# Kernel tuning notes

Hardware: AMD Instinct MI355X
Metric: run time of the kernel (lower is better)

Reference implementation:

```python
import jax, jax.numpy as jnp
import numpy as np
import math

N_LAYERS = 6
F = 512   # num_feature
H = 8     # num_head
DH = F // H
V = 32000 # vocab size
B = 64
S = 512   # == PositionalEncoding max_len
EPS = 1e-5


def _make_pe(max_len, d_model):
    position = np.arange(max_len, dtype=np.float32)[:, None]
    div_term = np.exp(np.arange(0, d_model, 2, dtype=np.float32) * (-math.log(10000.0) / d_model))
    pe = np.zeros((max_len, d_model), dtype=np.float32)
    pe[:, 0::2] = np.sin(position * div_term)
    pe[:, 1::2] = np.cos(position * div_term)
    return jnp.asarray(pe)


def setup_inputs() -> dict:
    key = jax.random.key(0)
    ks = jax.random.split(key, 16)
    w = lambda k, shape, s=0.02: (jax.random.normal(k, shape, dtype=jnp.float32) * s)
    inp = {
        "text": jax.random.randint(ks[0], (B, S), 0, V),
        "emb": jax.random.normal(ks[1], (V, F), dtype=jnp.float32) * 0.25,
        "pe": _make_pe(S, F),
        # per-layer params stacked on leading N axis
        "Wq": w(ks[2], (N_LAYERS, F, F)), "bq": jnp.zeros((N_LAYERS, F), jnp.float32),
        "Wk": w(ks[3], (N_LAYERS, F, F)), "bk": jnp.zeros((N_LAYERS, F), jnp.float32),
        "Wv": w(ks[4], (N_LAYERS, F, F)), "bv": jnp.zeros((N_LAYERS, F), jnp.float32),
        "g1": jnp.ones((N_LAYERS, F), jnp.float32), "beta1": jnp.zeros((N_LAYERS, F), jnp.float32),
        "Wf": w(ks[5], (N_LAYERS, F, F)), "bf": jnp.zeros((N_LAYERS, F), jnp.float32),
        "g2": jnp.ones((N_LAYERS, F), jnp.float32), "beta2": jnp.zeros((N_LAYERS, F), jnp.float32),
    }
    return inp


def _layernorm(x, g, b):
    m = jnp.mean(x, axis=-1, keepdims=True)
    v = jnp.mean(jnp.square(x - m), axis=-1, keepdims=True)
    return (x - m) * jax.lax.rsqrt(v + EPS) * g + b


def _encoder_layer(x, Wq, bq, Wk, bk, Wv, bv, g1, beta1, Wf, bf, g2, beta2):
    Bz, Sz, Fz = x.shape
    q = (x @ Wq + bq).reshape(Bz, Sz, H, DH)
    k = (x @ Wk + bk).reshape(Bz, Sz, H, DH)
    v = (x @ Wv + bv).reshape(Bz, Sz, H, DH)
    # FAITHFUL to source bug: attention over HEADS per token, no 1/sqrt(d) scaling.
    score = jnp.einsum('bshd,bsgd->bshg', q, k)          # [B,S,H,H]
    weight = jax.nn.softmax(score, axis=-1)
    attn = jnp.einsum('bshg,bsgd->bshd', weight, v).reshape(Bz, Sz, Fz)
    x = _layernorm(attn + x, g1, beta1)
    x = _layernorm((x @ Wf + bf) + x, g2, beta2)
    return x


def reference(text, emb, pe, Wq, bq, Wk, bk, Wv, bv, g1, beta1, Wf, bf, g2, beta2):
    x = emb[text] + pe[None, :text.shape[1], :]  # embedding + pos-enc (dropout = eval identity)
    for i in range(N_LAYERS):
        x = _encoder_layer(x, Wq[i], bq[i], Wk[i], bk[i], Wv[i], bv[i],
                           g1[i], beta1[i], Wf[i], bf[i], g2[i], beta2[i])
    return x
```

## Files before the change

### kernel.cpp

```cpp
#include <hip/hip_runtime.h>
#include <stdint.h>

typedef unsigned short u16;
using frag8 = __attribute__((ext_vector_type(8))) short;
using f32x4 = __attribute__((ext_vector_type(4))) float;

#define NTOK 32768
#define FDIM 512

__device__ __forceinline__ float bflo(uint32_t p){ union{uint32_t u; float f;} v; v.u = p<<16; return v.f; }
__device__ __forceinline__ float bfhi(uint32_t p){ union{uint32_t u; float f;} v; v.u = p & 0xffff0000u; return v.f; }
__device__ __forceinline__ float bf1(u16 x){ union{uint32_t u; float f;} v; v.u = ((uint32_t)x)<<16; return v.f; }
__device__ __forceinline__ u16 f2bf(float f){
  union{float f; uint32_t u;} v; v.f = f;
  uint32_t u = v.u;
  u += 0x7fffu + ((u>>16)&1u);
  return (u16)(u>>16);
}

__device__ __forceinline__ void async16(const void* g, void* l){
  __builtin_amdgcn_global_load_lds((const __attribute__((address_space(1))) uint32_t*)g,
                                   (__attribute__((address_space(3))) uint32_t*)l, 16, 0, 0);
}

__global__ __launch_bounds__(256) void embed_kernel(const int* __restrict__ text,
    const float* __restrict__ emb, const float* __restrict__ pe,
    u16* __restrict__ xb, const int tok0){
  const int gid = blockIdx.x*256 + threadIdx.x;
  const int base = gid*4;
  const int tl = base >> 9;
  const int f  = base & 511;
  const int tg = tl + tok0;
  const int s  = tg & 511;
  const int tok = text[tg];
  const float4 e4 = *(const float4*)(emb + (size_t)tok*FDIM + f);
  const float4 p4 = *(const float4*)(pe  + (size_t)s*FDIM + f);
  ushort4 ob;
  ob.x = f2bf(e4.x + p4.x);
  ob.y = f2bf(e4.y + p4.y);
  ob.z = f2bf(e4.z + p4.z);
  ob.w = f2bf(e4.w + p4.w);
  *(ushort4*)(xb + base) = ob;
}

__global__ __launch_bounds__(256) void transpose_w(const float* __restrict__ Wq,
    const float* __restrict__ Wk, const float* __restrict__ Wv, const float* __restrict__ Wf,
    u16* __restrict__ WT){
  const int gid = blockIdx.x*256 + threadIdx.x;
  const int n   = gid & 2047;
  const int k8  = (gid>>11) & 63;
  const int lay = gid >> 17;
  const float* src; int col;
  if      (n <  512){ src = Wq; col = n;      }
  else if (n < 1024){ src = Wk; col = n-512;  }
  else if (n < 1536){ src = Wv; col = n-1024; }
  else              { src = Wf; col = n-1536; }
  src += (size_t)lay*FDIM*FDIM;
  u16 vals[8] __attribute__((aligned(16)));
  #pragma unroll
  for (int i=0;i<8;i++) vals[i] = f2bf(src[(size_t)(k8*8+i)*FDIM + col]);
  *(int4*)(WT + ((size_t)lay*2048 + n)*FDIM + k8*8) = *(const int4*)vals;
}

template<int MODE>
__global__ __launch_bounds__(256, 3) void gemm128(
    const u16* __restrict__ A, const u16* __restrict__ BT,
    const float* __restrict__ b0, const float* __restrict__ b1, const float* __restrict__ b2,
    const u16* __restrict__ resid, u16* __restrict__ C, const int ldC, const int NB){
  __shared__ __attribute__((aligned(16))) short As[3*128*32];
  __shared__ __attribute__((aligned(16))) short Bs[3*128*32];
  const int nwg = gridDim.x;
  const int orig = blockIdx.x;
  const int wg = ((nwg & 7) == 0) ? ((orig & 7)*(nwg >> 3) + (orig >> 3)) : orig;
  const int nblk = wg % NB, mblk = wg / NB;
  const int m0 = mblk << 7, n0 = nblk << 7;
  const int tid = threadIdx.x;
  const int wid = tid >> 6, l = tid & 63;
  const int lm = l & 15, quad = l >> 4;

  const int srow = wid*16 + (l >> 2);
  const int sch  = (l & 3) ^ ((l >> 3) & 3);
  const char* Asrc0 = (const char*)A  + ((size_t)(m0 + srow))*1024 + sch*16;
  const char* Asrc1 = Asrc0 + 64*1024;
  const char* Bsrc0 = (const char*)BT + ((size_t)(n0 + srow))*1024 + sch*16;
  const char* Bsrc1 = Bsrc0 + 64*1024;
  char* ldsAw = (char*)As + wid*1024;
  char* ldsBw = (char*)Bs + wid*1024;

  f32x4 acc[4][4];
  #pragma unroll
  for (int i=0;i<4;i++)
    #pragma unroll
    for (int j=0;j<4;j++){ f32x4 z = {0.f,0.f,0.f,0.f}; acc[i][j] = z; }

  const int rsel = quad ^ ((lm >> 1) & 3);
  const int aB = ((wid>>1)*64 + lm)*32 + rsel*8;
  const int bB = ((wid&1)*64  + lm)*32 + rsel*8;

  #pragma unroll
  for (int kt=0; kt<2; kt++){
    async16(Asrc0 + kt*64, ldsAw + kt*8192);
    async16(Asrc1 + kt*64, ldsAw + kt*8192 + 4096);
    async16(Bsrc0 + kt*64, ldsBw + kt*8192);
    async16(Bsrc1 + kt*64, ldsBw + kt*8192 + 4096);
  }

#define TILE(T_, DOSTAGE, VMC) { \
    asm volatile("s_waitcnt vmcnt(" #VMC ")" ::: "memory"); \
    __builtin_amdgcn_s_barrier(); \
    asm volatile("" ::: "memory"); \
    if (DOSTAGE){ const int s_ = ((T_)+2)%3; const int off_ = ((T_)+2)*64; \
      async16(Asrc0 + off_, ldsAw + s_*8192); \
      async16(Asrc1 + off_, ldsAw + s_*8192 + 4096); } \
    const short* sA_ = As + ((T_)%3)*4096; \
    const short* sB_ = Bs + ((T_)%3)*4096; \
    frag8 af_[4], bf_[4]; \
    _Pragma("unroll") \
    for (int x_=0;x_<4;x_++) af_[x_] = *(const frag8*)(sA_ + aB + x_*512); \
    _Pragma("unroll") \
    for (int x_=0;x_<4;x_++) bf_[x_] = *(const frag8*)(sB_ + bB + x_*512); \
    if (DOSTAGE){ const int s_ = ((T_)+2)%3; const int off_ = ((T_)+2)*64; \
      async16(Bsrc0 + off_, ldsBw + s_*8192); \
      async16(Bsrc1 + off_, ldsBw + s_*8192 + 4096); } \
    __builtin_amdgcn_s_setprio(1); \
    _Pragma("unroll") \
    for (int mi_=0;mi_<4;mi_++) \
      _Pragma("unroll") \
      for (int nj_=0;nj_<4;nj_++) \
        acc[mi_][nj_] = __builtin_amdgcn_mfma_f32_16x16x32_bf16(af_[mi_], bf_[nj_], acc[mi_][nj_], 0,0,0); \
    __builtin_amdgcn_s_setprio(0); }

  TILE(0,1,4)  TILE(1,1,4)  TILE(2,1,4)  TILE(3,1,4)
  TILE(4,1,4)  TILE(5,1,4)  TILE(6,1,4)  TILE(7,1,4)
  TILE(8,1,4)  TILE(9,1,4)  TILE(10,1,4) TILE(11,1,4)
  TILE(12,1,4) TILE(13,1,4) TILE(14,0,4) TILE(15,0,0)
#undef TILE

  float bias[4]; int cols[4];
  #pragma unroll
  for (int nj=0;nj<4;nj++){
    const int c = n0 + (wid&1)*64 + nj*16 + lm;
    cols[nj] = c;
    if (MODE==0) bias[nj] = (c<512 ? b0[c] : (c<1024 ? b1[c-512] : b2[c-1024]));
    else         bias[nj] = b0[c];
  }
  #pragma unroll
  for (int mi=0; mi<4; mi++){
    const int rbase = m0 + (wid>>1)*64 + mi*16 + quad*4;
    #pragma unroll
    for (int r=0;r<4;r++){
      const size_t row = (size_t)(rbase + r);
      #pragma unroll
      for (int nj=0;nj<4;nj++){
        float v = acc[mi][nj][r] + bias[nj];
        if (MODE==1) v += bf1(resid[row*FDIM + cols[nj]]);
        C[row*(size_t)ldC + cols[nj]] = f2bf(v);
      }
    }
  }
}

__global__ __launch_bounds__(256) void attn_ln1(const u16* __restrict__ qkvb,
    const u16* __restrict__ xb, const float* __restrict__ gam, const float* __restrict__ bet,
    u16* __restrict__ y1b){
  __shared__ __attribute__((aligned(16))) u16 sQ[4][1536];
  __shared__ float sWt[4][64];
  const int tid = threadIdx.x, w = tid>>6, l = tid&63;
  const int t = blockIdx.x*4 + w;
  {
    const int4* src = (const int4*)(qkvb + (size_t)t*1536);
    int4* dst = (int4*)(&sQ[w][0]);
    #pragma unroll
    for (int i=0;i<3;i++) dst[i*64 + l] = src[i*64 + l];
  }
  __syncthreads();
  const int h = l>>3, g = l&7;
  const u16* qrow = &sQ[w][h*64];
  const u16* krow = &sQ[w][512 + g*64];
  float sc = 0.f;
  const int dstart = (l&31)*2;
  #pragma unroll
  for (int i=0;i<32;i++){
    const int d = (dstart + 2*i) & 63;
    const uint32_t qp = *(const uint32_t*)(qrow + d);
    const uint32_t kp = *(const uint32_t*)(krow + d);
    sc += bflo(qp)*bflo(kp) + bfhi(qp)*bfhi(kp);
  }
  float mx = sc;
  mx = fmaxf(mx, __shfl_xor(mx,1));
  mx = fmaxf(mx, __shfl_xor(mx,2));
  mx = fmaxf(mx, __shfl_xor(mx,4));
  const float e = __expf(sc - mx);
  float ssum = e;
  ssum += __shfl_xor(ssum,1);
  ssum += __shfl_xor(ssum,2);
  ssum += __shfl_xor(ssum,4);
  sWt[w][l] = e / ssum;
  __syncthreads();
  float wt[8];
  #pragma unroll
  for (int gg=0;gg<8;gg++) wt[gg] = sWt[w][h*8+gg];
  float att[8] = {0,0,0,0,0,0,0,0};
  const int d0 = (l&7)*8;
  #pragma unroll
  for (int gg=0;gg<8;gg++){
    const int4 vv = *(const int4*)(&sQ[w][1024 + gg*64 + d0]);
    const uint32_t* vp = (const uint32_t*)&vv;
    #pragma unroll
    for (int p=0;p<4;p++){
      att[2*p]   += wt[gg]*bflo(vp[p]);
      att[2*p+1] += wt[gg]*bfhi(vp[p]);
    }
  }
  const size_t rb = (size_t)t*FDIM + l*8;
  const int4 xv = *(const int4*)(xb + rb);
  const uint32_t* xp = (const uint32_t*)&xv;
  float y[8]; float s1=0.f, s2=0.f;
  #pragma unroll
  for (int p=0;p<4;p++){
    y[2*p]   = att[2*p]   + bflo(xp[p]);
    y[2*p+1] = att[2*p+1] + bfhi(xp[p]);
  }
  #pragma unroll
  for (int j=0;j<8;j++){ s1 += y[j]; s2 += y[j]*y[j]; }
  #pragma unroll
  for (int off=1; off<64; off<<=1){ s1 += __shfl_xor(s1,off); s2 += __shfl_xor(s2,off); }
  const float mean = s1*(1.f/512.f);
  const float var  = s2*(1.f/512.f) - mean*mean;
  const float rstd = rsqrtf(var + 1e-5f);
  const float4 g0 = *(const float4*)(gam + l*8);
  const float4 g1v = *(const float4*)(gam + l*8 + 4);
  const float4 b0v = *(const float4*)(bet + l*8);
  const float4 b1v = *(const float4*)(bet + l*8 + 4);
  float of[8];
  of[0]=(y[0]-mean)*rstd*g0.x + b0v.x;
  of[1]=(y[1]-mean)*rstd*g0.y + b0v.y;
  of[2]=(y[2]-mean)*rstd*g0.z + b0v.z;
  of[3]=(y[3]-mean)*rstd*g0.w + b0v.w;
  of[4]=(y[4]-mean)*rstd*g1v.x + b1v.x;
  of[5]=(y[5]-mean)*rstd*g1v.y + b1v.y;
  of[6]=(y[6]-mean)*rstd*g1v.z + b1v.z;
  of[7]=(y[7]-mean)*rstd*g1v.w + b1v.w;
  u16 ob[8] __attribute__((aligned(16)));
  #pragma unroll
  for (int j=0;j<8;j++) ob[j] = f2bf(of[j]);
  *(int4*)(y1b + rb) = *(const int4*)ob;
}

__global__ __launch_bounds__(256) void ln2_kernel(const u16* __restrict__ z,
    const float* __restrict__ gam, const float* __restrict__ bet,
    u16* __restrict__ xb, float* __restrict__ outp, const int final_){
  const int tid = threadIdx.x, w = tid>>6, l = tid&63;
  const int t = blockIdx.x*4 + w;
  const size_t rb = (size_t)t*FDIM + l*8;
  const int4 zv = *(const int4*)(z + rb);
  const uint32_t* zp = (const uint32_t*)&zv;
  float y[8];
  #pragma unroll
  for (int p=0;p<4;p++){ y[2*p]=bflo(zp[p]); y[2*p+1]=bfhi(zp[p]); }
  float s1=0.f, s2=0.f;
  #pragma unroll
  for (int j=0;j<8;j++){ s1+=y[j]; s2+=y[j]*y[j]; }
  #pragma unroll
  for (int off=1; off<64; off<<=1){ s1 += __shfl_xor(s1,off); s2 += __shfl_xor(s2,off); }
  const float mean = s1*(1.f/512.f);
  const float var  = s2*(1.f/512.f) - mean*mean;
  const float rstd = rsqrtf(var + 1e-5f);
  const float4 g0 = *(const float4*)(gam + l*8);
  const float4 g1v = *(const float4*)(gam + l*8 + 4);
  const float4 b0v = *(const float4*)(bet + l*8);
  const float4 b1v = *(const float4*)(bet + l*8 + 4);
  float of[8];
  of[0]=(y[0]-mean)*rstd*g0.x + b0v.x;
  of[1]=(y[1]-mean)*rstd*g0.y + b0v.y;
  of[2]=(y[2]-mean)*rstd*g0.z + b0v.z;
  of[3]=(y[3]-mean)*rstd*g0.w + b0v.w;
  of[4]=(y[4]-mean)*rstd*g1v.x + b1v.x;
  of[5]=(y[5]-mean)*rstd*g1v.y + b1v.y;
  of[6]=(y[6]-mean)*rstd*g1v.z + b1v.z;
  of[7]=(y[7]-mean)*rstd*g1v.w + b1v.w;
  if (final_){
    float4 o0; o0.x=of[0]; o0.y=of[1]; o0.z=of[2]; o0.w=of[3];
    float4 o1; o1.x=of[4]; o1.y=of[5]; o1.z=of[6]; o1.w=of[7];
    *(float4*)(outp + rb) = o0;
    *(float4*)(outp + rb + 4) = o1;
  } else {
    u16 ob[8] __attribute__((aligned(16)));
    #pragma unroll
    for (int j=0;j<8;j++) ob[j] = f2bf(of[j]);
    *(int4*)(xb + rb) = *(const int4*)ob;
  }
}

extern "C" void kernel_launch(void* const* d_in, const int* in_sizes, int n_in,
                              void* d_out, int out_size, void* d_ws, size_t ws_size,
                              hipStream_t stream){
  const int*   text = (const int*)d_in[0];
  const float* emb = (const float*)d_in[1];
  const float* pe  = (const float*)d_in[2];
  const float* Wq  = (const float*)d_in[3];
  const float* bq  = (const float*)d_in[4];
  const float* Wk  = (const float*)d_in[5];
  const float* bk  = (const float*)d_in[6];
  const float* Wv  = (const float*)d_in[7];
  const float* bv  = (const float*)d_in[8];
  const float* g1  = (const float*)d_in[9];
  const float* be1 = (const float*)d_in[10];
  const float* Wf  = (const float*)d_in[11];
  const float* bf_ = (const float*)d_in[12];
  const float* g2  = (const float*)d_in[13];
  const float* be2 = (const float*)d_in[14];
  float* outp = (float*)d_out;

  const size_t wtB = (size_t)6*2048*512*2;
  int T = NTOK;
  while (T > 2048 && wtB + (size_t)T*5120 > ws_size) T >>= 1;

  char* ws = (char*)d_ws;
  u16*   WT  = (u16*)ws;
  char*  act = ws + wtB;
  u16*   xb  = (u16*)act;
  u16*   y1b = (u16*)(act + (size_t)T*1024);
  u16*   qkv = (u16*)(act + (size_t)T*2048);
  u16*   zb  = qkv;

  hipLaunchKernelGGL(transpose_w, dim3(3072), dim3(256), 0, stream, Wq, Wk, Wv, Wf, WT);

  const int chunks = NTOK / T;
  for (int c = 0; c < chunks; c++){
    const int tok0 = c*T;
    hipLaunchKernelGGL(embed_kernel, dim3(T/2), dim3(256), 0, stream, text, emb, pe, xb, tok0);
    for (int lay=0; lay<6; lay++){
      const u16* WTl = WT + (size_t)lay*2048*FDIM;
      hipLaunchKernelGGL((gemm128<0>), dim3((T/128)*12), dim3(256), 0, stream,
          xb, WTl, bq + lay*FDIM, bk + lay*FDIM, bv + lay*FDIM, (const u16*)nullptr, qkv, 1536, 12);
      hipLaunchKernelGGL(attn_ln1, dim3(T/4), dim3(256), 0, stream,
          qkv, xb, g1 + lay*FDIM, be1 + lay*FDIM, y1b);
      hipLaunchKernelGGL((gemm128<1>), dim3((T/128)*4), dim3(256), 0, stream,
          y1b, WTl + (size_t)1536*FDIM, bf_ + lay*FDIM, (const float*)nullptr, (const float*)nullptr,
          y1b, zb, 512, 4);
      hipLaunchKernelGGL(ln2_kernel, dim3(T/4), dim3(256), 0, stream,
          zb, g2 + lay*FDIM, be2 + lay*FDIM, xb, outp + (size_t)tok0*FDIM, (lay==5)?1:0);
    }
  }
}
```

Baseline: 968.7 us.

## Replace 128x128 GEMM with 256x256 eight-wave ping-pong tiled kernel

Replaces the 128x128, 4-wave, triple-buffered GEMM with a 256x256 tile run by 512 threads (8 waves, each computing 128x64). It uses 128 KB of LDS double-buffered over K=64 steps, and interleaves quarter-tile LDS reads, async global-to-LDS staging and MFMA bursts between barriers. The larger tile raises arithmetic intensity and cuts global traffic per FLOP. The cost is more barriers, a larger LDS footprint limiting occupancy, and fewer workgroups for the N=512 GEMM (T/256*2 blocks), which may underfill the GPU.

Result: faster. 882.8 us (-8.9%).

```diff
diff --git a/kernel.cpp b/kernel.cpp
--- a/kernel.cpp
+++ b/kernel.cpp
@@ -63,90 +63,112 @@
 }
 
 template<int MODE>
-__global__ __launch_bounds__(256, 3) void gemm128(
+__global__ __launch_bounds__(512, 2) void gemm8p(
     const u16* __restrict__ A, const u16* __restrict__ BT,
     const float* __restrict__ b0, const float* __restrict__ b1, const float* __restrict__ b2,
     const u16* __restrict__ resid, u16* __restrict__ C, const int ldC, const int NB){
-  __shared__ __attribute__((aligned(16))) short As[3*128*32];
-  __shared__ __attribute__((aligned(16))) short Bs[3*128*32];
+  __shared__ __attribute__((aligned(16))) char lds[131072];
   const int nwg = gridDim.x;
   const int orig = blockIdx.x;
-  const int wg = ((nwg & 7) == 0) ? ((orig & 7)*(nwg >> 3) + (orig >> 3)) : orig;
+  const int wg = ((nwg & 7)==0) ? ((orig&7)*(nwg>>3) + (orig>>3)) : orig;
   const int nblk = wg % NB, mblk = wg / NB;
-  const int m0 = mblk << 7, n0 = nblk << 7;
+  const int m0 = mblk<<8, n0 = nblk<<8;
   const int tid = threadIdx.x;
-  const int wid = tid >> 6, l = tid & 63;
-  const int lm = l & 15, quad = l >> 4;
-
-  const int srow = wid*16 + (l >> 2);
-  const int sch  = (l & 3) ^ ((l >> 3) & 3);
-  const char* Asrc0 = (const char*)A  + ((size_t)(m0 + srow))*1024 + sch*16;
-  const char* Asrc1 = Asrc0 + 64*1024;
-  const char* Bsrc0 = (const char*)BT + ((size_t)(n0 + srow))*1024 + sch*16;
-  const char* Bsrc1 = Bsrc0 + 64*1024;
-  char* ldsAw = (char*)As + wid*1024;
-  char* ldsBw = (char*)Bs + wid*1024;
-
-  f32x4 acc[4][4];
-  #pragma unroll
-  for (int i=0;i<4;i++)
+  const int wid = tid>>6, l = tid&63;
+  const int lm = l&15, quad = l>>4;
+  const int wm = wid>>2, wn = wid&3;
+
+  const int cg = (l&3) ^ ((l>>3)&3);
+  const char* aSrc = (const char*)A  + ((size_t)(m0 + (wid>>2)*128 + (wid&3)*16 + (l>>2)))*1024 + cg*16;
+  const char* bSrc = (const char*)BT + ((size_t)(n0 + (wid>>1)*64  + (wid&1)*16 + (l>>2)))*1024 + cg*16;
+  char* ldsAs = lds + wid*1024;
+  char* ldsBs = lds + 65536 + wid*1024;
+
+#define STGA(kt, kw, mh) async16(aSrc + (mh)*65536 + (kt)*128 + (kw)*64, \
+                                 ldsAs + (((kt)&1)*32768) + (kw)*16384 + (mh)*8192)
+#define STGB(kt, kw, nh) async16(bSrc + (nh)*32768 + (kt)*128 + (kw)*64, \
+                                 ldsBs + (((kt)&1)*32768) + (kw)*16384 + (nh)*8192)
+
+  f32x4 acc[8][4];
+  #pragma unroll
+  for (int i=0;i<8;i++)
     #pragma unroll
     for (int j=0;j<4;j++){ f32x4 z = {0.f,0.f,0.f,0.f}; acc[i][j] = z; }
 
-  const int rsel = quad ^ ((lm >> 1) & 3);
-  const int aB = ((wid>>1)*64 + lm)*32 + rsel*8;
-  const int bB = ((wid&1)*64  + lm)*32 + rsel*8;
-
-  #pragma unroll
-  for (int kt=0; kt<2; kt++){
-    async16(Asrc0 + kt*64, ldsAw + kt*8192);
-    async16(Asrc1 + kt*64, ldsAw + kt*8192 + 4096);
-    async16(Bsrc0 + kt*64, ldsBw + kt*8192);
-    async16(Bsrc1 + kt*64, ldsBw + kt*8192 + 4096);
-  }
-
-#define TILE(T_, DOSTAGE, VMC) { \
-    asm volatile("s_waitcnt vmcnt(" #VMC ")" ::: "memory"); \
-    __builtin_amdgcn_s_barrier(); \
-    asm volatile("" ::: "memory"); \
-    if (DOSTAGE){ const int s_ = ((T_)+2)%3; const int off_ = ((T_)+2)*64; \
-      async16(Asrc0 + off_, ldsAw + s_*8192); \
-      async16(Asrc1 + off_, ldsAw + s_*8192 + 4096); } \
-    const short* sA_ = As + ((T_)%3)*4096; \
-    const short* sB_ = Bs + ((T_)%3)*4096; \
-    frag8 af_[4], bf_[4]; \
-    _Pragma("unroll") \
-    for (int x_=0;x_<4;x_++) af_[x_] = *(const frag8*)(sA_ + aB + x_*512); \
-    _Pragma("unroll") \
-    for (int x_=0;x_<4;x_++) bf_[x_] = *(const frag8*)(sB_ + bB + x_*512); \
-    if (DOSTAGE){ const int s_ = ((T_)+2)%3; const int off_ = ((T_)+2)*64; \
-      async16(Bsrc0 + off_, ldsBw + s_*8192); \
-      async16(Bsrc1 + off_, ldsBw + s_*8192 + 4096); } \
-    __builtin_amdgcn_s_setprio(1); \
-    _Pragma("unroll") \
-    for (int mi_=0;mi_<4;mi_++) \
-      _Pragma("unroll") \
-      for (int nj_=0;nj_<4;nj_++) \
-        acc[mi_][nj_] = __builtin_amdgcn_mfma_f32_16x16x32_bf16(af_[mi_], bf_[nj_], acc[mi_][nj_], 0,0,0); \
-    __builtin_amdgcn_s_setprio(0); }
-
-  TILE(0,1,4)  TILE(1,1,4)  TILE(2,1,4)  TILE(3,1,4)
-  TILE(4,1,4)  TILE(5,1,4)  TILE(6,1,4)  TILE(7,1,4)
-  TILE(8,1,4)  TILE(9,1,4)  TILE(10,1,4) TILE(11,1,4)
-  TILE(12,1,4) TILE(13,1,4) TILE(14,0,4) TILE(15,0,0)
-#undef TILE
+  const int csw = (quad ^ ((l>>1)&3))*16;
+  const char* aRd = lds + wm*4096 + lm*64 + csw;
+  const char* bRd = lds + 65536 + wn*2048 + lm*64 + csw;
+
+  frag8 a[4][2], bR[2][2][2];
+
+  STGA(0,0,0); STGA(0,1,0); STGB(0,0,0); STGB(0,1,0); STGB(0,0,1); STGB(0,1,1); STGA(0,0,1); STGA(0,1,1);
+  STGA(1,0,0); STGA(1,1,0); STGB(1,0,0); STGB(1,1,0); STGB(1,0,1); STGB(1,1,1);
+  asm volatile("s_waitcnt vmcnt(6)" ::: "memory");
+  __builtin_amdgcn_s_barrier();
+
+#define RDA(BUF, MH) { _Pragma("unroll") for (int mi_=0;mi_<4;mi_++){ \
+    a[mi_][0] = *(const frag8*)(aRd + (BUF)*32768 + (MH)*8192 + mi_*1024); \
+    a[mi_][1] = *(const frag8*)(aRd + (BUF)*32768 + 16384 + (MH)*8192 + mi_*1024); } }
+#define RDB(BUF, NH) { _Pragma("unroll") for (int nj_=0;nj_<2;nj_++){ \
+    bR[NH][nj_][0] = *(const frag8*)(bRd + (BUF)*32768 + (NH)*8192 + nj_*1024); \
+    bR[NH][nj_][1] = *(const frag8*)(bRd + (BUF)*32768 + 16384 + (NH)*8192 + nj_*1024); } }
+#define MM(MH, NH) { __builtin_amdgcn_s_setprio(1); \
+  _Pragma("unroll") for (int kw_=0;kw_<2;kw_++) \
+  _Pragma("unroll") for (int mi_=0;mi_<4;mi_++) \
+  _Pragma("unroll") for (int nj_=0;nj_<2;nj_++) \
+    acc[(MH)*4+mi_][(NH)*2+nj_] = __builtin_amdgcn_mfma_f32_16x16x32_bf16( \
+        a[mi_][kw_], bR[NH][nj_][kw_], acc[(MH)*4+mi_][(NH)*2+nj_], 0,0,0); \
+  __builtin_amdgcn_s_setprio(0); }
+#define BAR __builtin_amdgcn_s_barrier()
+
+#define ITER(T, FULL) { \
+   RDA(((T)&1),0); RDB(((T)&1),0); STGA((T)+1,0,1); STGA((T)+1,1,1); \
+           BAR; MM(0,0); BAR; \
+   RDB(((T)&1),1); if (FULL){ STGA((T)+2,0,0); STGA((T)+2,1,0); } \
+           BAR; MM(0,1); BAR; \
+   RDA(((T)&1),1); if (FULL){ STGB((T)+2,0,0); STGB((T)+2,1,0); } \
+           BAR; MM(1,0); BAR; \
+   if (FULL){ STGB((T)+2,0,1); STGB((T)+2,1,1); } \
+           BAR; MM(1,1); \
+           if (FULL){ asm volatile("s_waitcnt vmcnt(6)" ::: "memory"); } \
+           else     { asm volatile("s_waitcnt vmcnt(0)" ::: "memory"); } \
+           BAR; \
+   RDA((((T)+1)&1),0); RDB((((T)+1)&1),0); if (FULL){ STGA((T)+2,0,1); STGA((T)+2,1,1); } \
+           BAR; MM(0,0); BAR; \
+   RDB((((T)+1)&1),1); if (FULL){ STGA((T)+3,0,0); STGA((T)+3,1,0); } \
+           BAR; MM(0,1); BAR; \
+   RDA((((T)+1)&1),1); if (FULL){ STGB((T)+3,0,0); STGB((T)+3,1,0); } \
+           BAR; MM(1,0); BAR; \
+   if (FULL){ STGB((T)+3,0,1); STGB((T)+3,1,1); } \
+           BAR; MM(1,1); \
+           if (FULL){ asm volatile("s_waitcnt vmcnt(6)" ::: "memory"); } \
+           BAR; \
+}
+
+  ITER(0,1)
+  ITER(2,1)
+  ITER(4,1)
+  ITER(6,0)
+
+#undef ITER
+#undef BAR
+#undef MM
+#undef RDB
+#undef RDA
+#undef STGB
+#undef STGA
 
   float bias[4]; int cols[4];
   #pragma unroll
   for (int nj=0;nj<4;nj++){
-    const int c = n0 + (wid&1)*64 + nj*16 + lm;
+    const int c = n0 + wn*64 + nj*16 + lm;
     cols[nj] = c;
     if (MODE==0) bias[nj] = (c<512 ? b0[c] : (c<1024 ? b1[c-512] : b2[c-1024]));
     else         bias[nj] = b0[c];
   }
   #pragma unroll
-  for (int mi=0; mi<4; mi++){
-    const int rbase = m0 + (wid>>1)*64 + mi*16 + quad*4;
+  for (int mi=0; mi<8; mi++){
+    const int rbase = m0 + wm*128 + mi*16 + quad*4;
     #pragma unroll
     for (int r=0;r<4;r++){
       const size_t row = (size_t)(rbase + r);
@@ -332,13 +354,13 @@
     hipLaunchKernelGGL(embed_kernel, dim3(T/2), dim3(256), 0, stream, text, emb, pe, xb, tok0);
     for (int lay=0; lay<6; lay++){
       const u16* WTl = WT + (size_t)lay*2048*FDIM;
-      hipLaunchKernelGGL((gemm128<0>), dim3((T/128)*12), dim3(256), 0, stream,
-          xb, WTl, bq + lay*FDIM, bk + lay*FDIM, bv + lay*FDIM, (const u16*)nullptr, qkv, 1536, 12);
+      hipLaunchKernelGGL((gemm8p<0>), dim3((T/256)*6), dim3(512), 0, stream,
+          xb, WTl, bq + lay*FDIM, bk + lay*FDIM, bv + lay*FDIM, (const u16*)nullptr, qkv, 1536, 6);
       hipLaunchKernelGGL(attn_ln1, dim3(T/4), dim3(256), 0, stream,
           qkv, xb, g1 + lay*FDIM, be1 + lay*FDIM, y1b);
-      hipLaunchKernelGGL((gemm128<1>), dim3((T/128)*4), dim3(256), 0, stream,
+      hipLaunchKernelGGL((gemm8p<1>), dim3((T/256)*2), dim3(512), 0, stream,
           y1b, WTl + (size_t)1536*FDIM, bf_ + lay*FDIM, (const float*)nullptr, (const float*)nullptr,
-          y1b, zb, 512, 4);
+          y1b, zb, 512, 2);
       hipLaunchKernelGGL(ln2_kernel, dim3(T/4), dim3(256), 0, stream,
           zb, g2 + lay*FDIM, be2 + lay*FDIM, xb, outp + (size_t)tok0*FDIM, (lay==5)?1:0);
     }
```
